# Performance work log

Hardware: AMD Instinct MI355X
Metric: run time of the kernel (lower is better)

## Reference

```python
import jax, jax.numpy as jnp
import numpy as np

B, L, P, C = 8, 4, 1024, 256
NH, NS = 8, 4
HD = C // NH  # 32
LEVEL_HW = [(64, 64), (32, 32), (16, 16), (8, 8)]


def setup_inputs() -> dict:
    key = jax.random.key(0)
    ks = jax.random.split(key, 14)
    inp = {
        "x": jax.random.normal(ks[0], (B, L, P, C), jnp.float32),
        # reference points are grid_sample coords in [-1, 1]
        "ref": jax.random.uniform(ks[1], (B, L, P, 2), jnp.float32, -0.9, 0.9),
    }
    for i, (h, w) in enumerate(LEVEL_HW):
        inp[f"feat{i}"] = jax.random.normal(ks[2 + i], (B, C, h, w), jnp.float32)
    inp["w_attn"] = jax.random.normal(ks[6], (C, NH * NS), jnp.float32) * 0.02
    inp["b_attn"] = jax.random.normal(ks[7], (NH * NS,), jnp.float32) * 0.02
    inp["w_off"] = jax.random.normal(ks[8], (C, 2 * NH * NS), jnp.float32) * 0.02
    inp["b_off"] = jax.random.normal(ks[9], (2 * NH * NS,), jnp.float32) * 0.02
    inp["embed_w"] = jax.random.normal(ks[10], (L, C, HD), jnp.float32) * 0.02
    inp["embed_b"] = jax.random.normal(ks[11], (L, HD), jnp.float32) * 0.02
    return inp


def grid_sample_bilinear(feat, grid):
    """torch.F.grid_sample(mode='bilinear', padding_mode='zeros', align_corners=True).
    feat: (B, C, H, W); grid: (B, Gh, Gw, 2) with (x, y) in [-1, 1].
    Returns (B, Gh, Gw, C)  (already permuted vs torch's (B, C, Gh, Gw))."""
    Bn, Cn, H, W = feat.shape
    fx = (grid[..., 0] + 1.0) * 0.5 * (W - 1)  # align_corners=True mapping
    fy = (grid[..., 1] + 1.0) * 0.5 * (H - 1)
    x0f = jnp.floor(fx)
    y0f = jnp.floor(fy)
    x0 = x0f.astype(jnp.int32)
    y0 = y0f.astype(jnp.int32)
    x1 = x0 + 1
    y1 = y0 + 1
    wx1 = fx - x0f
    wy1 = fy - y0f
    wx0 = 1.0 - wx1
    wy0 = 1.0 - wy1
    feat_hwc = jnp.transpose(feat, (0, 2, 3, 1))  # (B, H, W, C)

    def gather(yi, xi):
        valid = ((yi >= 0) & (yi < H) & (xi >= 0) & (xi < W)).astype(feat.dtype)
        yc = jnp.clip(yi, 0, H - 1)
        xc = jnp.clip(xi, 0, W - 1)
        v = jax.vmap(lambda f, y, x: f[y, x])(feat_hwc, yc, xc)  # (B, Gh, Gw, C)
        return v * valid[..., None]

    out = (gather(y0, x0) * (wy0 * wx0)[..., None]
           + gather(y0, x1) * (wy0 * wx1)[..., None]
           + gather(y1, x0) * (wy1 * wx0)[..., None]
           + gather(y1, x1) * (wy1 * wx1)[..., None])
    return out


def reference(x, ref, feat0, feat1, feat2, feat3,
              w_attn, b_attn, w_off, b_off, embed_w, embed_b):
    feats = [feat0, feat1, feat2, feat3]
    b, l, p, c = x.shape
    # attention weights: softmax over samples
    weights = jax.nn.softmax((x @ w_attn + b_attn).reshape(b, l, p, NH, NS), axis=-1)
    # sampling offsets, squashed by tanh
    offsets = jnp.tanh((x @ w_off + b_off).reshape(b, l, p, NH * NS, 2))
    pos = offsets + ref[:, :, :, None, :]  # (b, l, p, NH*NS, 2)
    sampled = []
    for i, f in enumerate(feats):
        s = grid_sample_bilinear(f, pos[:, i])  # (b, p, NH*NS, C_l)
        sampled.append(s @ embed_w[i] + embed_b[i])  # (b, p, NH*NS, HD)
    fs = jnp.stack(sampled, axis=1).reshape(b, l, p, NH, NS, HD)
    out = (weights[..., None] * fs).sum(axis=-2).reshape(b, l, p, NH * HD)
    return out
```

## Files before the change

kernel.cpp:

```cpp
#include <hip/hip_runtime.h>
#include <math.h>

#define B_   8
#define L_   4
#define P_   1024
#define C_   256
#define NH_  8
#define NS_  4
#define HD_  32

typedef _Float16 half8 __attribute__((ext_vector_type(8)));
typedef float    f32x4 __attribute__((ext_vector_type(4)));

#define G_F     0u
#define SAMP_F  1392640u

__constant__ const int kGoff[4] = {0, 1048576, 1310720, 1376256};

#define XH  136
#define LGS 100
#define NG_GPROJ 680

__global__ __launch_bounds__(256) void stage1(
    const float* __restrict__ f0, const float* __restrict__ f1,
    const float* __restrict__ f2, const float* __restrict__ f3,
    const float* __restrict__ embed_w, _Float16* __restrict__ g16,
    const float* __restrict__ x,
    const float* __restrict__ ref,
    const float* __restrict__ wa, const float* __restrict__ ba,
    const float* __restrict__ wo, const float* __restrict__ bo,
    float4* __restrict__ samp4)
{
  __shared__ float4 smraw4[2720];
  const int t = threadIdx.x;
  const int bx = blockIdx.x;

  if (bx < NG_GPROJ) {
    float* eL = (float*)smraw4;
    float (*fl)[64] = (float(*)[64])(eL + C_ * HD_);
    const int b = bx / 85;
    int sub = bx - b * 85, l, tile;
    const float* src;
    if (sub < 64)      { l = 0; tile = sub;      src = f0; }
    else if (sub < 80) { l = 1; tile = sub - 64; src = f1; }
    else if (sub < 84) { l = 2; tile = sub - 80; src = f2; }
    else               { l = 3; tile = 0;        src = f3; }
    const int Wl = 64 >> l, S = Wl * Wl;
    const int s0 = tile * 64;

    const float* E = embed_w + (size_t)l * (C_ * HD_);
    #pragma unroll
    for (int q = 0; q < 32; ++q) eL[q * 256 + t] = E[q * 256 + t];

    const float* sb = src + (size_t)b * C_ * S + s0;
    const int sl = t & 63, dg = t >> 6;
    float acc[8];
    #pragma unroll
    for (int e = 0; e < 8; ++e) acc[e] = 0.f;

    for (int c0 = 0; c0 < 256; c0 += 32) {
      __syncthreads();
      #pragma unroll
      for (int q = 0; q < 8; ++q) {
        const int e = q * 256 + t;
        fl[e >> 6][e & 63] = sb[(size_t)(c0 + (e >> 6)) * S + (e & 63)];
      }
      __syncthreads();
      #pragma unroll 8
      for (int ci = 0; ci < 32; ++ci) {
        const float f = fl[ci][sl];
        const float4* ep = (const float4*)&eL[(c0 + ci) * 32 + dg * 8];
        const float4 e0 = ep[0], e1 = ep[1];
        acc[0] += f * e0.x; acc[1] += f * e0.y; acc[2] += f * e0.z; acc[3] += f * e0.w;
        acc[4] += f * e1.x; acc[5] += f * e1.y; acc[6] += f * e1.z; acc[7] += f * e1.w;
      }
    }
    _Float16* gd = g16 + kGoff[l] + ((size_t)b * S + s0 + sl) * 32 + dg * 8;
    const half8 hv = {(_Float16)acc[0], (_Float16)acc[1], (_Float16)acc[2], (_Float16)acc[3],
                      (_Float16)acc[4], (_Float16)acc[5], (_Float16)acc[6], (_Float16)acc[7]};
    *(half8*)gd = hv;
    return;
  }

  _Float16* smx = (_Float16*)smraw4;
  _Float16* smw = (_Float16*)smraw4 + 64 * XH;
  float*    lg  = (float*)smraw4;

  const int blk = bx - NG_GPROJ;
  const int lane = t & 63, w = t >> 6;
  const int lr = lane & 15, kg = lane >> 4;
  const int gp0 = blk * 64;

  f32x4 acc[6];
  #pragma unroll
  for (int nt = 0; nt < 6; ++nt) acc[nt] = (f32x4){0.f, 0.f, 0.f, 0.f};

  #pragma unroll
  for (int chunk = 0; chunk < 2; ++chunk) {
    const int c0 = chunk * 128;
    if (chunk) __syncthreads();
    {
      const int pt = t >> 2, q = t & 3;
      const float4* src = (const float4*)(x + (size_t)(gp0 + pt) * 256 + c0 + q * 32);
      _Float16* dst = smx + pt * XH + q * 32;
      #pragma unroll
      for (int i = 0; i < 4; ++i) {
        const float4 v0 = src[2 * i], v1 = src[2 * i + 1];
        half8 h = {(_Float16)v0.x, (_Float16)v0.y, (_Float16)v0.z, (_Float16)v0.w,
                   (_Float16)v1.x, (_Float16)v1.y, (_Float16)v1.z, (_Float16)v1.w};
        *(half8*)(dst + i * 8) = h;
      }
    }
    {
      const float4* wa4 = (const float4*)(wa + c0 * 32);
      #pragma unroll
      for (int q = 0; q < 4; ++q) {
        const int la = (q * 256 + t) * 4;
        const float4 v = wa4[q * 256 + t];
        const int cc = la >> 5, n = la & 31;
        smw[(n + 0) * XH + cc] = (_Float16)v.x;
        smw[(n + 1) * XH + cc] = (_Float16)v.y;
        smw[(n + 2) * XH + cc] = (_Float16)v.z;
        smw[(n + 3) * XH + cc] = (_Float16)v.w;
      }
      const float4* wo4 = (const float4*)(wo + c0 * 64);
      #pragma unroll
      for (int q = 0; q < 8; ++q) {
        const int la = (q * 256 + t) * 4;
        const float4 v = wo4[q * 256 + t];
        const int cc = la >> 6, n = 32 + (la & 63);
        smw[(n + 0) * XH + cc] = (_Float16)v.x;
        smw[(n + 1) * XH + cc] = (_Float16)v.y;
        smw[(n + 2) * XH + cc] = (_Float16)v.z;
        smw[(n + 3) * XH + cc] = (_Float16)v.w;
      }
    }
    __syncthreads();

    #pragma unroll
    for (int ks = 0; ks < 4; ++ks) {
      const half8 a = *(const half8*)(smx + (w * 16 + lr) * XH + ks * 32 + kg * 8);
      #pragma unroll
      for (int nt = 0; nt < 6; ++nt) {
        const half8 bf = *(const half8*)(smw + (nt * 16 + lr) * XH + ks * 32 + kg * 8);
        acc[nt] = __builtin_amdgcn_mfma_f32_16x16x32_f16(a, bf, acc[nt], 0, 0, 0);
      }
    }
  }
  __syncthreads();

  #pragma unroll
  for (int nt = 0; nt < 6; ++nt) {
    const int n = nt * 16 + lr;
    const float bv = (n < 32) ? ba[n] : bo[n - 32];
    #pragma unroll
    for (int r = 0; r < 4; ++r)
      lg[(w * 16 + kg * 4 + r) * LGS + n] = acc[nt][r] + bv;
  }
  __syncthreads();

  #pragma unroll
  for (int k = 0; k < 8; ++k) {
    const int slot = k * 256 + t;
    const int pp = slot >> 5, j = slot & 31;
    const int gp = gp0 + pp;
    const int l = (gp >> 10) & 3;
    const int Wl = 64 >> l;
    const float* lgp = lg + pp * LGS;
    const int h4 = (j >> 2) * 4;
    const float l0 = lgp[h4], l1 = lgp[h4 + 1], l2 = lgp[h4 + 2], l3 = lgp[h4 + 3];
    const float m = fmaxf(fmaxf(l0, l1), fmaxf(l2, l3));
    const float e0 = expf(l0 - m), e1 = expf(l1 - m), e2 = expf(l2 - m), e3 = expf(l3 - m);
    const float inv = 1.f / (e0 + e1 + e2 + e3);
    const float es[4] = {e0, e1, e2, e3};
    const float wj = es[j & 3] * inv;
    const float ox = tanhf(lgp[32 + 2 * j])     + ref[(size_t)gp * 2];
    const float oy = tanhf(lgp[32 + 2 * j + 1]) + ref[(size_t)gp * 2 + 1];
    const float sc = 0.5f * (float)(Wl - 1);
    samp4[(size_t)gp * 32 + j] = make_float4(wj, (ox + 1.f) * sc, (oy + 1.f) * sc, 0.f);
  }
}

__global__ __launch_bounds__(256) void k3_main(
    const _Float16* __restrict__ g16,
    const float4* __restrict__ samp4,
    const float* __restrict__ embed_b,
    float* __restrict__ out)
{
  __shared__ int4   tofs[256];
  __shared__ float4 tws[256];
  const int t = threadIdx.x, blk = blockIdx.x;
  const int gp0 = blk * 8;
  const int l = (gp0 >> 10) & 3, b = gp0 >> 12;
  const int Wl = 64 >> l;
  const int gbase = kGoff[l] + b * Wl * Wl * 32;

  {
    const float4 s = samp4[(size_t)gp0 * 32 + t];
    const float fx = s.y, fy = s.z;
    const float x0f = floorf(fx), y0f = floorf(fy);
    const int x0 = (int)x0f, y0 = (int)y0f, x1 = x0 + 1, y1 = y0 + 1;
    const float wx1 = fx - x0f, wy1 = fy - y0f;
    const float wx0 = 1.f - wx1, wy0 = 1.f - wy1;
    const float xv0 = (x0 >= 0 && x0 < Wl) ? 1.f : 0.f;
    const float xv1 = (x1 >= 0 && x1 < Wl) ? 1.f : 0.f;
    const float yv0 = (y0 >= 0 && y0 < Wl) ? 1.f : 0.f;
    const float yv1 = (y1 >= 0 && y1 < Wl) ? 1.f : 0.f;
    const int x0c = min(max(x0, 0), Wl - 1), x1c = min(max(x1, 0), Wl - 1);
    const int y0c = min(max(y0, 0), Wl - 1), y1c = min(max(y1, 0), Wl - 1);
    tofs[t] = make_int4(gbase + (y0c * Wl + x0c) * 32,
                        gbase + (y0c * Wl + x1c) * 32,
                        gbase + (y1c * Wl + x0c) * 32,
                        gbase + (y1c * Wl + x1c) * 32);
    const float w = s.x;
    tws[t] = make_float4(w * wy0 * wx0 * yv0 * xv0,
                         w * wy0 * wx1 * yv0 * xv1,
                         w * wy1 * wx0 * yv1 * xv0,
                         w * wy1 * wx1 * yv1 * xv1);
  }
  __syncthreads();

  const int dq = t & 3, h = (t >> 2) & 7, pt = t >> 5;
  float a[8];
  {
    const float4* bb = (const float4*)(embed_b + l * 32 + dq * 8);
    const float4 b0 = bb[0], b1 = bb[1];
    a[0] = b0.x; a[1] = b0.y; a[2] = b0.z; a[3] = b0.w;
    a[4] = b1.x; a[5] = b1.y; a[6] = b1.z; a[7] = b1.w;
  }
  #pragma unroll
  for (int s = 0; s < 4; ++s) {
    const int slot = pt * 32 + h * 4 + s;
    const int4   o = tofs[slot];
    const float4 w = tws[slot];
    const half8 v00 = *(const half8*)(g16 + o.x + dq * 8);
    const half8 v01 = *(const half8*)(g16 + o.y + dq * 8);
    const half8 v10 = *(const half8*)(g16 + o.z + dq * 8);
    const half8 v11 = *(const half8*)(g16 + o.w + dq * 8);
    #pragma unroll
    for (int j = 0; j < 8; ++j)
      a[j] += w.x * (float)v00[j] + w.y * (float)v01[j]
            + w.z * (float)v10[j] + w.w * (float)v11[j];
  }
  float* od = out + (size_t)(gp0 + pt) * 256 + h * 32 + dq * 8;
  ((float4*)od)[0] = make_float4(a[0], a[1], a[2], a[3]);
  ((float4*)od)[1] = make_float4(a[4], a[5], a[6], a[7]);
}

extern "C" void kernel_launch(void* const* d_in, const int* in_sizes, int n_in,
                              void* d_out, int out_size, void* d_ws, size_t ws_size,
                              hipStream_t stream) {
  const float* x      = (const float*)d_in[0];
  const float* ref    = (const float*)d_in[1];
  const float* w_attn = (const float*)d_in[6];
  const float* b_attn = (const float*)d_in[7];
  const float* w_off  = (const float*)d_in[8];
  const float* b_off  = (const float*)d_in[9];
  const float* emb_w  = (const float*)d_in[10];
  const float* emb_b  = (const float*)d_in[11];
  float* ws  = (float*)d_ws;
  float* out = (float*)d_out;

  _Float16* g16   = (_Float16*)(ws + G_F);
  float4*   samp4 = (float4*)(ws + SAMP_F);

  stage1<<<NG_GPROJ + B_ * L_ * P_ / 64, 256, 0, stream>>>(
      (const float*)d_in[2], (const float*)d_in[3],
      (const float*)d_in[4], (const float*)d_in[5], emb_w, g16,
      x, ref, w_attn, b_attn, w_off, b_off, samp4);

  k3_main<<<B_ * L_ * P_ / 8, 256, 0, stream>>>(g16, samp4, emb_b, out);
}
```

Measured before the change: 58.89 us.

## Pre-convert projection and embed weights to fp16 once; shrink shared memory in stage1

Adds a small pre-kernel that converts the attention/offset weights (transposed) and the embedding weights to fp16 once per call, instead of every stage1 block redoing the fp32 loads, conversions and scattered transposed LDS stores. The gproj path now keeps embed weights and feature tiles in fp16 shared memory, and the projection path uses 64-wide K chunks, so the LDS footprint drops and occupancy can rise. The cost is an extra kernel launch, an extra small workspace round trip, and fp16 rounding of the feature values in the gproj accumulation.

```diff
diff --git a/kernel.cpp b/kernel.cpp
--- a/kernel.cpp
+++ b/kernel.cpp
@@ -10,34 +10,53 @@
 #define HD_  32
 
 typedef _Float16 half8 __attribute__((ext_vector_type(8)));
+typedef _Float16 half4 __attribute__((ext_vector_type(4)));
 typedef float    f32x4 __attribute__((ext_vector_type(4)));
 
 #define G_F     0u
 #define SAMP_F  1392640u
+#define WU_F    5586944u
+#define E16_F   5611520u
 
 __constant__ const int kGoff[4] = {0, 1048576, 1310720, 1376256};
 
-#define XH  136
+#define XH2 72
 #define LGS 100
 #define NG_GPROJ 680
+
+__global__ void k0_conv(const float* __restrict__ wa, const float* __restrict__ wo,
+                        const float* __restrict__ embed_w,
+                        _Float16* __restrict__ WuT, _Float16* __restrict__ E16) {
+  const int bx = blockIdx.x, t = threadIdx.x;
+  if (bx < 96) {
+    const int n = bx;
+    const float v = (n < 32) ? wa[t * 32 + n] : wo[t * 64 + (n - 32)];
+    WuT[n * 256 + t] = (_Float16)v;
+  } else {
+    const int i0 = (bx - 96) * 1024 + t * 4;
+    const float4 v = *(const float4*)(embed_w + i0);
+    *(half4*)(E16 + i0) = (half4){(_Float16)v.x, (_Float16)v.y,
+                                  (_Float16)v.z, (_Float16)v.w};
+  }
+}
 
 __global__ __launch_bounds__(256) void stage1(
     const float* __restrict__ f0, const float* __restrict__ f1,
     const float* __restrict__ f2, const float* __restrict__ f3,
-    const float* __restrict__ embed_w, _Float16* __restrict__ g16,
+    const _Float16* __restrict__ E16, _Float16* __restrict__ g16,
     const float* __restrict__ x,
     const float* __restrict__ ref,
-    const float* __restrict__ wa, const float* __restrict__ ba,
-    const float* __restrict__ wo, const float* __restrict__ bo,
+    const _Float16* __restrict__ WuT,
+    const float* __restrict__ ba, const float* __restrict__ bo,
     float4* __restrict__ samp4)
 {
-  __shared__ float4 smraw4[2720];
+  __shared__ float4 smraw4[1600];
   const int t = threadIdx.x;
   const int bx = blockIdx.x;
 
   if (bx < NG_GPROJ) {
-    float* eL = (float*)smraw4;
-    float (*fl)[64] = (float(*)[64])(eL + C_ * HD_);
+    _Float16* eL = (_Float16*)smraw4;
+    _Float16* fl = eL + 256 * 32;
     const int b = bx / 85;
     int sub = bx - b * 85, l, tile;
     const float* src;
@@ -48,9 +67,12 @@
     const int Wl = 64 >> l, S = Wl * Wl;
     const int s0 = tile * 64;
 
-    const float* E = embed_w + (size_t)l * (C_ * HD_);
-    #pragma unroll
-    for (int q = 0; q < 32; ++q) eL[q * 256 + t] = E[q * 256 + t];
+    {
+      const float4* es = (const float4*)(E16 + (size_t)l * 8192);
+      float4* ed = (float4*)eL;
+      #pragma unroll
+      for (int q = 0; q < 4; ++q) ed[q * 256 + t] = es[q * 256 + t];
+    }
 
     const float* sb = src + (size_t)b * C_ * S + s0;
     const int sl = t & 63, dg = t >> 6;
@@ -63,16 +85,15 @@
       #pragma unroll
       for (int q = 0; q < 8; ++q) {
         const int e = q * 256 + t;
-        fl[e >> 6][e & 63] = sb[(size_t)(c0 + (e >> 6)) * S + (e & 63)];
+        fl[(e >> 6) * 64 + (e & 63)] = (_Float16)sb[(size_t)(c0 + (e >> 6)) * S + (e & 63)];
       }
       __syncthreads();
       #pragma unroll 8
       for (int ci = 0; ci < 32; ++ci) {
-        const float f = fl[ci][sl];
-        const float4* ep = (const float4*)&eL[(c0 + ci) * 32 + dg * 8];
-        const float4 e0 = ep[0], e1 = ep[1];
-        acc[0] += f * e0.x; acc[1] += f * e0.y; acc[2] += f * e0.z; acc[3] += f * e0.w;
-        acc[4] += f * e1.x; acc[5] += f * e1.y; acc[6] += f * e1.z; acc[7] += f * e1.w;
+        const float f = (float)fl[ci * 64 + sl];
+        const half8 ev = *(const half8*)(eL + (c0 + ci) * 32 + dg * 8);
+        #pragma unroll
+        for (int e = 0; e < 8; ++e) acc[e] += f * (float)ev[e];
       }
     }
     _Float16* gd = g16 + kGoff[l] + ((size_t)b * S + s0 + sl) * 32 + dg * 8;
@@ -83,7 +104,7 @@
   }
 
   _Float16* smx = (_Float16*)smraw4;
-  _Float16* smw = (_Float16*)smraw4 + 64 * XH;
+  _Float16* smw = (_Float16*)smraw4 + 64 * XH2;
   float*    lg  = (float*)smraw4;
 
   const int blk = bx - NG_GPROJ;
@@ -96,53 +117,36 @@
   for (int nt = 0; nt < 6; ++nt) acc[nt] = (f32x4){0.f, 0.f, 0.f, 0.f};
 
   #pragma unroll
-  for (int chunk = 0; chunk < 2; ++chunk) {
-    const int c0 = chunk * 128;
+  for (int chunk = 0; chunk < 4; ++chunk) {
+    const int c0 = chunk * 64;
     if (chunk) __syncthreads();
     {
       const int pt = t >> 2, q = t & 3;
-      const float4* src = (const float4*)(x + (size_t)(gp0 + pt) * 256 + c0 + q * 32);
-      _Float16* dst = smx + pt * XH + q * 32;
-      #pragma unroll
-      for (int i = 0; i < 4; ++i) {
-        const float4 v0 = src[2 * i], v1 = src[2 * i + 1];
-        half8 h = {(_Float16)v0.x, (_Float16)v0.y, (_Float16)v0.z, (_Float16)v0.w,
-                   (_Float16)v1.x, (_Float16)v1.y, (_Float16)v1.z, (_Float16)v1.w};
-        *(half8*)(dst + i * 8) = h;
-      }
+      const float4* src = (const float4*)(x + (size_t)(gp0 + pt) * 256 + c0 + q * 16);
+      const float4 v0 = src[0], v1 = src[1], v2 = src[2], v3 = src[3];
+      _Float16* dst = smx + pt * XH2 + q * 16;
+      *(half8*)dst = (half8){(_Float16)v0.x, (_Float16)v0.y, (_Float16)v0.z, (_Float16)v0.w,
+                             (_Float16)v1.x, (_Float16)v1.y, (_Float16)v1.z, (_Float16)v1.w};
+      *(half8*)(dst + 8) = (half8){(_Float16)v2.x, (_Float16)v2.y, (_Float16)v2.z, (_Float16)v2.w,
+                                   (_Float16)v3.x, (_Float16)v3.y, (_Float16)v3.z, (_Float16)v3.w};
     }
     {
-      const float4* wa4 = (const float4*)(wa + c0 * 32);
-      #pragma unroll
-      for (int q = 0; q < 4; ++q) {
-        const int la = (q * 256 + t) * 4;
-        const float4 v = wa4[q * 256 + t];
-        const int cc = la >> 5, n = la & 31;
-        smw[(n + 0) * XH + cc] = (_Float16)v.x;
-        smw[(n + 1) * XH + cc] = (_Float16)v.y;
-        smw[(n + 2) * XH + cc] = (_Float16)v.z;
-        smw[(n + 3) * XH + cc] = (_Float16)v.w;
-      }
-      const float4* wo4 = (const float4*)(wo + c0 * 64);
-      #pragma unroll
-      for (int q = 0; q < 8; ++q) {
-        const int la = (q * 256 + t) * 4;
-        const float4 v = wo4[q * 256 + t];
-        const int cc = la >> 6, n = 32 + (la & 63);
-        smw[(n + 0) * XH + cc] = (_Float16)v.x;
-        smw[(n + 1) * XH + cc] = (_Float16)v.y;
-        smw[(n + 2) * XH + cc] = (_Float16)v.z;
-        smw[(n + 3) * XH + cc] = (_Float16)v.w;
+      #pragma unroll
+      for (int q = 0; q < 3; ++q) {
+        const int idx = q * 256 + t;
+        const int n = idx >> 3, col8 = idx & 7;
+        *(float4*)(smw + n * XH2 + col8 * 8) =
+            *(const float4*)(WuT + (size_t)n * 256 + c0 + col8 * 8);
       }
     }
     __syncthreads();
 
     #pragma unroll
-    for (int ks = 0; ks < 4; ++ks) {
-      const half8 a = *(const half8*)(smx + (w * 16 + lr) * XH + ks * 32 + kg * 8);
+    for (int ks = 0; ks < 2; ++ks) {
+      const half8 a = *(const half8*)(smx + (w * 16 + lr) * XH2 + ks * 32 + kg * 8);
       #pragma unroll
       for (int nt = 0; nt < 6; ++nt) {
-        const half8 bf = *(const half8*)(smw + (nt * 16 + lr) * XH + ks * 32 + kg * 8);
+        const half8 bf = *(const half8*)(smw + (nt * 16 + lr) * XH2 + ks * 32 + kg * 8);
         acc[nt] = __builtin_amdgcn_mfma_f32_16x16x32_f16(a, bf, acc[nt], 0, 0, 0);
       }
     }
@@ -263,11 +267,15 @@
 
   _Float16* g16   = (_Float16*)(ws + G_F);
   float4*   samp4 = (float4*)(ws + SAMP_F);
+  _Float16* WuT   = (_Float16*)(ws + WU_F);
+  _Float16* E16   = (_Float16*)(ws + E16_F);
+
+  k0_conv<<<128, 256, 0, stream>>>(w_attn, w_off, emb_w, WuT, E16);
 
   stage1<<<NG_GPROJ + B_ * L_ * P_ / 64, 256, 0, stream>>>(
       (const float*)d_in[2], (const float*)d_in[3],
-      (const float*)d_in[4], (const float*)d_in[5], emb_w, g16,
-      x, ref, w_attn, b_attn, w_off, b_off, samp4);
+      (const float*)d_in[4], (const float*)d_in[5], E16, g16,
+      x, ref, WuT, b_attn, b_off, samp4);
 
   k3_main<<<B_ * L_ * P_ / 8, 256, 0, stream>>>(g16, samp4, emb_b, out);
 }
```

New measurement: 61.74 us. 4.8% more time.
